# Performance work log

Measured on AMD Instinct MI355X. Metric: run time of the kernel, lower is better.

Reference implementation:

```python
import jax, jax.numpy as jnp
import numpy as np

N_NODES = 100000


def _gcn_layer(x, W, b, row, col, norm, n_nodes):
    # x: [N, Fin], W: [Fin, Fout]. GCN: A_hat @ (x W) + b with symmetric norm.
    xw = x @ W                                   # [N, Fout]
    msg = xw[row] * norm[:, None]                # [E+N, Fout] gathered messages
    agg = jax.ops.segment_sum(msg, col, num_segments=n_nodes)  # scatter-add at dst
    return agg + b


def setup_inputs() -> dict:
    key = jax.random.key(0)
    ks = jax.random.split(key, 5)
    N, E = N_NODES, 1600000
    Fin, F1, F2, C = 512, 64, 128, 40
    x = jax.random.normal(ks[0], (N, Fin), dtype=jnp.float32)
    edge_index = jax.random.randint(ks[1], (2, E), 0, N, dtype=jnp.int64)
    W1 = jax.random.normal(ks[2], (Fin, F1), dtype=jnp.float32) / np.sqrt(Fin)
    W2 = jax.random.normal(ks[3], (F1, F2), dtype=jnp.float32) / np.sqrt(F1)
    W3 = jax.random.normal(ks[4], (F2, C), dtype=jnp.float32) / np.sqrt(F2)
    return {
        "x": x, "edge_index": edge_index,
        "W1": W1, "b1": jnp.zeros((F1,), jnp.float32),
        "W2": W2, "b2": jnp.zeros((F2,), jnp.float32),
        "W3": W3, "b3": jnp.zeros((C,), jnp.float32),
    }


def reference(x, edge_index, W1, b1, W2, b2, W3, b3):
    N = x.shape[0]
    # Add self-loops (GCNConv default add_self_loops=True)
    loop = jnp.arange(N, dtype=edge_index.dtype)
    row = jnp.concatenate([edge_index[0], loop])  # source nodes
    col = jnp.concatenate([edge_index[1], loop])  # destination nodes
    # Symmetric degree normalization: deg computed at destination with self-loops
    deg = jax.ops.segment_sum(jnp.ones_like(col, dtype=x.dtype), col, num_segments=N)
    dis = jax.lax.rsqrt(deg)                      # deg >= 1 due to self-loops
    norm = dis[row] * dis[col]                    # [E+N]

    h1 = jax.nn.relu(_gcn_layer(x, W1, b1, row, col, norm, N))
    # dropout is identity (training=False)
    h2 = jax.nn.relu(_gcn_layer(h1, W2, b2, row, col, norm, N))
    h3 = _gcn_layer(h2, W3, b3, row, col, norm, N)
    return jax.nn.log_softmax(h3, axis=1)
```

## Files before the change

### kernel.cpp

```cpp
#include <hip/hip_runtime.h>
#include <math.h>


typedef __attribute__((ext_vector_type(8))) short short8;
typedef __attribute__((ext_vector_type(4))) float f32x4;

__device__ __forceinline__ unsigned short f2bf(float f) {
    unsigned int u = __float_as_uint(f);
    unsigned int r = (u + 0x7fffu + ((u >> 16) & 1u)) >> 16;
    return (unsigned short)r;
}
__device__ __forceinline__ float bflo(unsigned int u) { return __uint_as_float(u << 16); }
__device__ __forceinline__ float bfhi(unsigned int u) { return __uint_as_float(u & 0xffff0000u); }

__device__ __forceinline__ void wprep_one(const float* W, unsigned short* out,
                                          int KS, int FOUT, int t) {
    int i = t & 7;
    int l = (t >> 3) & 63;
    int g = t >> 9;
    int ks = g % KS;
    int nt = g / KS;
    int k = ks * 32 + (l >> 4) * 8 + i;
    int c = nt * 16 + (l & 15);
    out[t] = (c < FOUT) ? f2bf(W[(size_t)k * FOUT + c]) : (unsigned short)0;
}

__global__ void prep_kernel(const float* __restrict__ W1, const float* __restrict__ W2,
                            const float* __restrict__ W3,
                            unsigned short* __restrict__ Wf1, unsigned short* __restrict__ Wf2,
                            unsigned short* __restrict__ Wf3,
                            int* __restrict__ cnt, int* __restrict__ fillc, int N) {
    int t = blockIdx.x * 256 + threadIdx.x;
    if (t < 32768)       wprep_one(W1, Wf1, 16, 64, t);
    else if (t < 40960)  wprep_one(W2, Wf2, 2, 128, t - 32768);
    else if (t < 47104)  wprep_one(W3, Wf3, 4, 40, t - 40960);
    if (t < N) cnt[t] = 0;
    else if (t < 2 * N) fillc[t - N] = 0;
}

__global__ void count_kernel(const int* __restrict__ col, int* __restrict__ cnt, int E) {
    int e = blockIdx.x * 256 + threadIdx.x;
    if (e < E) atomicAdd(&cnt[col[e]], 1);
}

__global__ void scan1_kernel(const int* __restrict__ cnt, int* __restrict__ out,
                             int* __restrict__ bsums, int n) {
    __shared__ int s[1024];
    int i = blockIdx.x * 1024 + threadIdx.x;
    int v = (i < n) ? cnt[i] : 0;
    s[threadIdx.x] = v;
    __syncthreads();
    for (int off = 1; off < 1024; off <<= 1) {
        int t = 0;
        if ((int)threadIdx.x >= off) t = s[threadIdx.x - off];
        __syncthreads();
        if ((int)threadIdx.x >= off) s[threadIdx.x] += t;
        __syncthreads();
    }
    if (i < n) out[i] = s[threadIdx.x] - v;
    if (threadIdx.x == 1023) bsums[blockIdx.x] = s[1023];
}

__global__ void scan2_kernel(int* bsums, int nb) {
    __shared__ int s[128];
    int v = ((int)threadIdx.x < nb) ? bsums[threadIdx.x] : 0;
    s[threadIdx.x] = v;
    __syncthreads();
    for (int off = 1; off < 128; off <<= 1) {
        int t = 0;
        if ((int)threadIdx.x >= off) t = s[threadIdx.x - off];
        __syncthreads();
        if ((int)threadIdx.x >= off) s[threadIdx.x] += t;
        __syncthreads();
    }
    if ((int)threadIdx.x < nb) bsums[threadIdx.x] = s[threadIdx.x] - v;
}

__global__ void scan3d_kernel(int* __restrict__ ptr, const int* __restrict__ bsums,
                              const int* __restrict__ cnt, float* __restrict__ dis,
                              int n, int E) {
    int i = blockIdx.x * 1024 + threadIdx.x;
    if (i < n) {
        ptr[i] += bsums[blockIdx.x];
        dis[i] = rsqrtf((float)(cnt[i] + 1));
    }
    if (i == 0) ptr[n] = E;
}

__global__ void fill_kernel(const int* __restrict__ row, const int* __restrict__ col,
                            const int* __restrict__ ptr, int* __restrict__ fillc,
                            const float* __restrict__ dis, uint2* __restrict__ csr_en, int E) {
    int e = blockIdx.x * 256 + threadIdx.x;
    if (e < E) {
        int c = col[e];
        int r = row[e];
        int p = ptr[c] + atomicAdd(&fillc[c], 1);
        uint2 en;
        en.x = (unsigned int)r;
        en.y = __float_as_uint(dis[r] * dis[c]);
        csr_en[p] = en;
    }
}

__global__ __launch_bounds__(256) void gemm1_kernel(const float* __restrict__ Ap,
                                                    const unsigned short* __restrict__ Wf,
                                                    unsigned short* __restrict__ Y, int N) {
    __shared__ float red[3][64][17];
    const int lane = threadIdx.x & 63;
    const int wid = threadIdx.x >> 6;
    const int rbase = blockIdx.x * 16;
    const int rA = rbase + (lane & 15);
    const bool va = rA < N;
    const int khalf = lane >> 4;
    const float* base = Ap + (size_t)rA * 512 + wid * 128 + khalf * 8;

    float4 x0[4], x1[4];
#pragma unroll
    for (int s = 0; s < 4; s++) {
        const float4* arow = (const float4*)(base + s * 32);
        if (va) { x0[s] = arow[0]; x1[s] = arow[1]; }
        else    { x0[s] = make_float4(0, 0, 0, 0); x1[s] = x0[s]; }
    }

    f32x4 acc[4];
#pragma unroll
    for (int nt = 0; nt < 4; nt++)
#pragma unroll
        for (int j = 0; j < 4; j++) acc[nt][j] = 0.f;

#pragma unroll
    for (int s = 0; s < 4; s++) {
        short8 afr;
        afr[0] = (short)f2bf(x0[s].x); afr[1] = (short)f2bf(x0[s].y);
        afr[2] = (short)f2bf(x0[s].z); afr[3] = (short)f2bf(x0[s].w);
        afr[4] = (short)f2bf(x1[s].x); afr[5] = (short)f2bf(x1[s].y);
        afr[6] = (short)f2bf(x1[s].z); afr[7] = (short)f2bf(x1[s].w);
        const int ks = wid * 4 + s;
#pragma unroll
        for (int nt = 0; nt < 4; nt++) {
            short8 bfr = *(const short8*)(Wf + (((size_t)nt * 16 + ks) * 64 + lane) * 8);
            acc[nt] = __builtin_amdgcn_mfma_f32_16x16x32_bf16(afr, bfr, acc[nt], 0, 0, 0);
        }
    }

    if (wid > 0) {
#pragma unroll
        for (int nt = 0; nt < 4; nt++)
#pragma unroll
            for (int j = 0; j < 4; j++)
                red[wid - 1][lane][nt * 4 + j] = acc[nt][j];
    }
    __syncthreads();
    if (wid == 0) {
#pragma unroll
        for (int nt = 0; nt < 4; nt++)
#pragma unroll
            for (int j = 0; j < 4; j++) {
                float v = acc[nt][j];
                v += red[0][lane][nt * 4 + j];
                v += red[1][lane][nt * 4 + j];
                v += red[2][lane][nt * 4 + j];
                acc[nt][j] = v;
            }
        const int rD0 = rbase + (lane >> 4) * 4;
        const int colb = lane & 15;
#pragma unroll
        for (int nt = 0; nt < 4; nt++) {
            int c = nt * 16 + colb;
#pragma unroll
            for (int i = 0; i < 4; i++) {
                int rD = rD0 + i;
                if (rD < N) Y[(size_t)rD * 64 + c] = f2bf(acc[nt][i]);
            }
        }
    }
}

__global__ __launch_bounds__(256) void gemm23_kernel(const unsigned short* __restrict__ A,
                                                     const unsigned short* __restrict__ Wf2,
                                                     const float* __restrict__ b2,
                                                     const unsigned short* __restrict__ Wf3,
                                                     unsigned short* __restrict__ Y, int N) {
    __shared__ unsigned short hs[4][16][136];
    const int lane = threadIdx.x & 63;
    const int wid = threadIdx.x >> 6;
    const int rbase = blockIdx.x * 64 + wid * 16;
    const int rA = rbase + (lane & 15);
    const bool va = rA < N;
    const int khalf = lane >> 4;

    f32x4 acc2[8];
#pragma unroll
    for (int nt = 0; nt < 8; nt++)
#pragma unroll
        for (int j = 0; j < 4; j++) acc2[nt][j] = 0.f;

#pragma unroll
    for (int ks = 0; ks < 2; ks++) {
        short8 afr;
        if (va) afr = *(const short8*)(A + (size_t)rA * 64 + ks * 32 + khalf * 8);
        else {
#pragma unroll
            for (int j = 0; j < 8; j++) afr[j] = 0;
        }
#pragma unroll
        for (int nt = 0; nt < 8; nt++) {
            short8 bfr = *(const short8*)(Wf2 + (((size_t)nt * 2 + ks) * 64 + lane) * 8);
            acc2[nt] = __builtin_amdgcn_mfma_f32_16x16x32_bf16(afr, bfr, acc2[nt], 0, 0, 0);
        }
    }

    const int rD = (lane >> 4) * 4;
    const int colb = lane & 15;
#pragma unroll
    for (int nt = 0; nt < 8; nt++) {
        int c = nt * 16 + colb;
        float bv = b2[c];
#pragma unroll
        for (int j = 0; j < 4; j++)
            hs[wid][rD + j][c] = f2bf(fmaxf(acc2[nt][j] + bv, 0.f));
    }
    __syncthreads();

    f32x4 acc3[3];
#pragma unroll
    for (int nt = 0; nt < 3; nt++)
#pragma unroll
        for (int j = 0; j < 4; j++) acc3[nt][j] = 0.f;

    const int r = lane & 15;
#pragma unroll
    for (int ks = 0; ks < 4; ks++) {
        short8 afr = *(const short8*)&hs[wid][r][ks * 32 + khalf * 8];
#pragma unroll
        for (int nt = 0; nt < 3; nt++) {
            short8 bfr = *(const short8*)(Wf3 + (((size_t)nt * 4 + ks) * 64 + lane) * 8);
            acc3[nt] = __builtin_amdgcn_mfma_f32_16x16x32_bf16(afr, bfr, acc3[nt], 0, 0, 0);
        }
    }

#pragma unroll
    for (int nt = 0; nt < 3; nt++) {
        int c = nt * 16 + colb;
        if (c < 40) {
#pragma unroll
            for (int i = 0; i < 4; i++) {
                int rr = rbase + rD + i;
                if (rr < N) Y[(size_t)rr * 40 + c] = f2bf(acc3[nt][i]);
            }
        }
    }
}

template <bool BR>
__global__ __launch_bounds__(256) void agg64_kernel(const unsigned int* __restrict__ XW,
                                                    const float* __restrict__ bias,
                                                    const int* __restrict__ ptr,
                                                    const uint2* __restrict__ EN,
                                                    unsigned int* __restrict__ Y, int N) {
    const int lane = threadIdx.x & 63;
    const int wid = threadIdx.x >> 6;
    const int n = blockIdx.x * 4 + wid;
    if (n >= N) return;
    const int s = lane >> 3;
    const int q = lane & 7;

    const int e0 = ptr[n], e1 = ptr[n + 1];
    const float selfw = 1.0f / (float)(e1 - e0 + 1);

    float acc[8];
    if (s == 0) {
        const uint4 u = *(const uint4*)(XW + (size_t)n * 32 + q * 4);
        acc[0] = selfw * bflo(u.x); acc[1] = selfw * bfhi(u.x);
        acc[2] = selfw * bflo(u.y); acc[3] = selfw * bfhi(u.y);
        acc[4] = selfw * bflo(u.z); acc[5] = selfw * bfhi(u.z);
        acc[6] = selfw * bflo(u.w); acc[7] = selfw * bfhi(u.w);
    } else {
#pragma unroll
        for (int j = 0; j < 8; j++) acc[j] = 0.f;
    }

    for (int eb = e0; eb < e1; eb += 64) {
        int cnt = e1 - eb; if (cnt > 64) cnt = 64;
        uint2 en;
        if (lane < cnt) en = EN[eb + lane];
        else { en.x = 0; en.y = 0; }
#pragma unroll 2
        for (int k = s; k < cnt; k += 8) {
            int r = __shfl((int)en.x, k);
            float nrm = __uint_as_float((unsigned int)__shfl((int)en.y, k));
            const uint4 u = *(const uint4*)(XW + (size_t)r * 32 + q * 4);
            acc[0] += nrm * bflo(u.x); acc[1] += nrm * bfhi(u.x);
            acc[2] += nrm * bflo(u.y); acc[3] += nrm * bfhi(u.y);
            acc[4] += nrm * bflo(u.z); acc[5] += nrm * bfhi(u.z);
            acc[6] += nrm * bflo(u.w); acc[7] += nrm * bfhi(u.w);
        }
    }

#pragma unroll
    for (int off = 8; off < 64; off <<= 1)
#pragma unroll
        for (int j = 0; j < 8; j++) acc[j] += __shfl_xor(acc[j], off);

    if (lane < 8) {
        float v[8];
        if (BR) {
            const float4 b0 = *((const float4*)bias + lane * 2);
            const float4 b1 = *((const float4*)bias + lane * 2 + 1);
            v[0] = fmaxf(acc[0] + b0.x, 0.f); v[1] = fmaxf(acc[1] + b0.y, 0.f);
            v[2] = fmaxf(acc[2] + b0.z, 0.f); v[3] = fmaxf(acc[3] + b0.w, 0.f);
            v[4] = fmaxf(acc[4] + b1.x, 0.f); v[5] = fmaxf(acc[5] + b1.y, 0.f);
            v[6] = fmaxf(acc[6] + b1.z, 0.f); v[7] = fmaxf(acc[7] + b1.w, 0.f);
        } else {
#pragma unroll
            for (int j = 0; j < 8; j++) v[j] = acc[j];
        }
        uint4 o;
        o.x = (unsigned int)f2bf(v[0]) | ((unsigned int)f2bf(v[1]) << 16);
        o.y = (unsigned int)f2bf(v[2]) | ((unsigned int)f2bf(v[3]) << 16);
        o.z = (unsigned int)f2bf(v[4]) | ((unsigned int)f2bf(v[5]) << 16);
        o.w = (unsigned int)f2bf(v[6]) | ((unsigned int)f2bf(v[7]) << 16);
        *(uint4*)(Y + (size_t)n * 32 + lane * 4) = o;
    }
}

__global__ __launch_bounds__(256) void agg40lsm_kernel(const unsigned int* __restrict__ XW,
                                                       const float* __restrict__ bias,
                                                       const int* __restrict__ ptr,
                                                       const uint2* __restrict__ EN,
                                                       float* __restrict__ out, int N) {
    const int lane = threadIdx.x & 63;
    const int wid = threadIdx.x >> 6;
    const int n = blockIdx.x * 4 + wid;
    if (n >= N) return;
    const int s = lane >> 4;
    const int c = lane & 15;
    const bool act = (c < 10);

    const int e0 = ptr[n], e1 = ptr[n + 1];
    const float selfw = 1.0f / (float)(e1 - e0 + 1);

    float acc[4] = {0.f, 0.f, 0.f, 0.f};
    if (s == 0 && act) {
        const uint2 u = *(const uint2*)(XW + (size_t)n * 20 + c * 2);
        acc[0] = selfw * bflo(u.x); acc[1] = selfw * bfhi(u.x);
        acc[2] = selfw * bflo(u.y); acc[3] = selfw * bfhi(u.y);
    }

    for (int eb = e0; eb < e1; eb += 64) {
        int cnt = e1 - eb; if (cnt > 64) cnt = 64;
        uint2 en;
        if (lane < cnt) en = EN[eb + lane];
        else { en.x = 0; en.y = 0; }
#pragma unroll 2
        for (int k = s; k < cnt; k += 4) {
            int r = __shfl((int)en.x, k);
            float nrm = __uint_as_float((unsigned int)__shfl((int)en.y, k));
            if (act) {
                const uint2 u = *(const uint2*)(XW + (size_t)r * 20 + c * 2);
                acc[0] += nrm * bflo(u.x); acc[1] += nrm * bfhi(u.x);
                acc[2] += nrm * bflo(u.y); acc[3] += nrm * bfhi(u.y);
            }
        }
    }

#pragma unroll
    for (int off = 16; off < 64; off <<= 1)
#pragma unroll
        for (int j = 0; j < 4; j++) acc[j] += __shfl_xor(acc[j], off);

    float v[4];
    float m = -INFINITY;
    if (lane < 16 && act) {
        const float4 b = *((const float4*)bias + c);
        v[0] = acc[0] + b.x; v[1] = acc[1] + b.y;
        v[2] = acc[2] + b.z; v[3] = acc[3] + b.w;
        m = fmaxf(fmaxf(v[0], v[1]), fmaxf(v[2], v[3]));
    }
#pragma unroll
    for (int off = 32; off; off >>= 1) m = fmaxf(m, __shfl_xor(m, off));
    float ex = 0.f;
    if (lane < 16 && act)
        ex = expf(v[0] - m) + expf(v[1] - m) + expf(v[2] - m) + expf(v[3] - m);
#pragma unroll
    for (int off = 32; off; off >>= 1) ex += __shfl_xor(ex, off);
    float ls = logf(ex);
    if (lane < 16 && act) {
        float4 o;
        o.x = v[0] - m - ls; o.y = v[1] - m - ls;
        o.z = v[2] - m - ls; o.w = v[3] - m - ls;
        *(float4*)(out + (size_t)n * 40 + c * 4) = o;
    }
}


extern "C" void kernel_launch(void* const* d_in, const int* in_sizes, int n_in,
                              void* d_out, int out_size, void* d_ws, size_t ws_size,
                              hipStream_t stream) {
    const float* x  = (const float*)d_in[0];
    const int*   ei = (const int*)d_in[1];
    const float* W1 = (const float*)d_in[2];
    const float* b1 = (const float*)d_in[3];
    const float* W2 = (const float*)d_in[4];
    const float* b2 = (const float*)d_in[5];
    const float* W3 = (const float*)d_in[6];
    const float* b3 = (const float*)d_in[7];
    const int N = in_sizes[0] / 512;
    const int E = in_sizes[1] / 2;
    const int* row = ei;
    const int* col = ei + E;

    char* p = (char*)d_ws;
    auto alloc = [&](size_t bytes) {
        void* r = (void*)p;
        p += (bytes + 255) & ~(size_t)255;
        return r;
    };
    float* dis    = (float*)alloc((size_t)N * 4);
    int*   cnt    = (int*)alloc((size_t)N * 4);
    int*   ptr    = (int*)alloc((size_t)(N + 1) * 4);
    int*   fillc  = (int*)alloc((size_t)N * 4);
    int*   bsums  = (int*)alloc(1024);
    uint2* csr_en = (uint2*)alloc((size_t)E * 8);
    unsigned short* Wf1 = (unsigned short*)alloc(4 * 16 * 64 * 8 * 2);
    unsigned short* Wf2 = (unsigned short*)alloc(8 * 2 * 64 * 8 * 2);
    unsigned short* Wf3 = (unsigned short*)alloc(3 * 4 * 64 * 8 * 2);
    unsigned short* xw1 = (unsigned short*)alloc((size_t)N * 64 * 2);
    unsigned short* h1  = (unsigned short*)alloc((size_t)N * 64 * 2);
    unsigned short* a2  = (unsigned short*)alloc((size_t)N * 64 * 2);
    unsigned short* xw3 = (unsigned short*)alloc((size_t)N * 40 * 2);
    float* out = (float*)d_out;

    prep_kernel<<<(2 * N + 255) / 256, 256, 0, stream>>>(W1, W2, W3, Wf1, Wf2, Wf3,
                                                         cnt, fillc, N);

    const int cgrid = (E + 255) / 256;
    count_kernel<<<cgrid, 256, 0, stream>>>(col, cnt, E);

    gemm1_kernel<<<(N + 15) / 16, 256, 0, stream>>>(x, Wf1, xw1, N);

    int nb = (N + 1023) / 1024;
    scan1_kernel<<<nb, 1024, 0, stream>>>(cnt, ptr, bsums, N);
    scan2_kernel<<<1, 128, 0, stream>>>(bsums, nb);
    scan3d_kernel<<<nb, 1024, 0, stream>>>(ptr, bsums, cnt, dis, N, E);
    fill_kernel<<<cgrid, 256, 0, stream>>>(row, col, ptr, fillc, dis, csr_en, E);

    const int ngrid = (N + 3) / 4;
    const int ggrid = (N + 63) / 64;

    agg64_kernel<true><<<ngrid, 256, 0, stream>>>((const unsigned int*)xw1, b1, ptr, csr_en,
                                                  (unsigned int*)h1, N);
    agg64_kernel<false><<<ngrid, 256, 0, stream>>>((const unsigned int*)h1, nullptr, ptr, csr_en,
                                                   (unsigned int*)a2, N);
    gemm23_kernel<<<ggrid, 256, 0, stream>>>(a2, Wf2, b2, Wf3, xw3, N);
    agg40lsm_kernel<<<ngrid, 256, 0, stream>>>((const unsigned int*)xw3, b3, ptr, csr_en, out, N);
}
```

Before: 374.6 us.

## Restructure gemm1 to stage 64-row bf16 tiles in LDS with double buffering

The first-layer GEMM previously split K across four waves per 16-row block and reduced partial sums through shared memory. It now gives each block 64 rows, one 16-row slice per wave over the full K. Each K chunk of x is loaded with coalesced float4 reads, converted to bf16 and stored in a double-buffered LDS tile. This removes the cross-wave reduction and reuses each W fragment across more rows, at the cost of more LDS traffic and a barrier per chunk.

```diff
diff --git a/kernel.cpp b/kernel.cpp
--- a/kernel.cpp
+++ b/kernel.cpp
@@ -105,22 +105,13 @@
 __global__ __launch_bounds__(256) void gemm1_kernel(const float* __restrict__ Ap,
                                                     const unsigned short* __restrict__ Wf,
                                                     unsigned short* __restrict__ Y, int N) {
-    __shared__ float red[3][64][17];
-    const int lane = threadIdx.x & 63;
-    const int wid = threadIdx.x >> 6;
-    const int rbase = blockIdx.x * 16;
-    const int rA = rbase + (lane & 15);
-    const bool va = rA < N;
+    __shared__ unsigned short As[2][64][136];
+    const int t = threadIdx.x;
+    const int lane = t & 63;
+    const int wid = t >> 6;
+    const int rbase = blockIdx.x * 64;
+    const int fr = lane & 15;
     const int khalf = lane >> 4;
-    const float* base = Ap + (size_t)rA * 512 + wid * 128 + khalf * 8;
-
-    float4 x0[4], x1[4];
-#pragma unroll
-    for (int s = 0; s < 4; s++) {
-        const float4* arow = (const float4*)(base + s * 32);
-        if (va) { x0[s] = arow[0]; x1[s] = arow[1]; }
-        else    { x0[s] = make_float4(0, 0, 0, 0); x1[s] = x0[s]; }
-    }
 
     f32x4 acc[4];
 #pragma unroll
@@ -128,50 +119,48 @@
 #pragma unroll
         for (int j = 0; j < 4; j++) acc[nt][j] = 0.f;
 
-#pragma unroll
-    for (int s = 0; s < 4; s++) {
-        short8 afr;
-        afr[0] = (short)f2bf(x0[s].x); afr[1] = (short)f2bf(x0[s].y);
-        afr[2] = (short)f2bf(x0[s].z); afr[3] = (short)f2bf(x0[s].w);
-        afr[4] = (short)f2bf(x1[s].x); afr[5] = (short)f2bf(x1[s].y);
-        afr[6] = (short)f2bf(x1[s].z); afr[7] = (short)f2bf(x1[s].w);
-        const int ks = wid * 4 + s;
-#pragma unroll
-        for (int nt = 0; nt < 4; nt++) {
-            short8 bfr = *(const short8*)(Wf + (((size_t)nt * 16 + ks) * 64 + lane) * 8);
-            acc[nt] = __builtin_amdgcn_mfma_f32_16x16x32_bf16(afr, bfr, acc[nt], 0, 0, 0);
-        }
-    }
-
-    if (wid > 0) {
-#pragma unroll
-        for (int nt = 0; nt < 4; nt++)
-#pragma unroll
-            for (int j = 0; j < 4; j++)
-                red[wid - 1][lane][nt * 4 + j] = acc[nt][j];
-    }
+    auto stage = [&](int buf, int c) {
+#pragma unroll
+        for (int rd = 0; rd < 8; rd++) {
+            int u = t + rd * 256;
+            int row = u >> 5;
+            int q = u & 31;
+            int gr = rbase + row; if (gr > N - 1) gr = N - 1;
+            float4 v = *(const float4*)(Ap + (size_t)gr * 512 + c * 128 + q * 4);
+            uint2 w;
+            w.x = (unsigned int)f2bf(v.x) | ((unsigned int)f2bf(v.y) << 16);
+            w.y = (unsigned int)f2bf(v.z) | ((unsigned int)f2bf(v.w) << 16);
+            *(uint2*)&As[buf][row][q * 4] = w;
+        }
+    };
+
+    stage(0, 0);
     __syncthreads();
-    if (wid == 0) {
-#pragma unroll
-        for (int nt = 0; nt < 4; nt++)
-#pragma unroll
-            for (int j = 0; j < 4; j++) {
-                float v = acc[nt][j];
-                v += red[0][lane][nt * 4 + j];
-                v += red[1][lane][nt * 4 + j];
-                v += red[2][lane][nt * 4 + j];
-                acc[nt][j] = v;
+#pragma unroll
+    for (int c = 0; c < 4; c++) {
+        if (c < 3) stage((c + 1) & 1, c + 1);
+#pragma unroll
+        for (int ks = 0; ks < 4; ks++) {
+            short8 afr = *(const short8*)&As[c & 1][wid * 16 + fr][ks * 32 + khalf * 8];
+            const int ksg = c * 4 + ks;
+#pragma unroll
+            for (int nt = 0; nt < 4; nt++) {
+                short8 bfr = *(const short8*)(Wf + (((size_t)nt * 16 + ksg) * 64 + lane) * 8);
+                acc[nt] = __builtin_amdgcn_mfma_f32_16x16x32_bf16(afr, bfr, acc[nt], 0, 0, 0);
             }
-        const int rD0 = rbase + (lane >> 4) * 4;
-        const int colb = lane & 15;
-#pragma unroll
-        for (int nt = 0; nt < 4; nt++) {
-            int c = nt * 16 + colb;
-#pragma unroll
-            for (int i = 0; i < 4; i++) {
-                int rD = rD0 + i;
-                if (rD < N) Y[(size_t)rD * 64 + c] = f2bf(acc[nt][i]);
-            }
+        }
+        __syncthreads();
+    }
+
+    const int rD0 = rbase + wid * 16 + (lane >> 4) * 4;
+    const int colb = lane & 15;
+#pragma unroll
+    for (int nt = 0; nt < 4; nt++) {
+        int c = nt * 16 + colb;
+#pragma unroll
+        for (int i = 0; i < 4; i++) {
+            int rD = rD0 + i;
+            if (rD < N) Y[(size_t)rD * 64 + c] = f2bf(acc[nt][i]);
         }
     }
 }
@@ -437,7 +426,8 @@
     const int cgrid = (E + 255) / 256;
     count_kernel<<<cgrid, 256, 0, stream>>>(col, cnt, E);
 
-    gemm1_kernel<<<(N + 15) / 16, 256, 0, stream>>>(x, Wf1, xw1, N);
+    const int ggrid = (N + 63) / 64;
+    gemm1_kernel<<<ggrid, 256, 0, stream>>>(x, Wf1, xw1, N);
 
     int nb = (N + 1023) / 1024;
     scan1_kernel<<<nb, 1024, 0, stream>>>(cnt, ptr, bsums, N);
@@ -446,7 +436,6 @@
     fill_kernel<<<cgrid, 256, 0, stream>>>(row, col, ptr, fillc, dis, csr_en, E);
 
     const int ngrid = (N + 3) / 4;
-    const int ggrid = (N + 63) / 64;
 
     agg64_kernel<true><<<ngrid, 256, 0, stream>>>((const unsigned int*)xw1, b1, ptr, csr_en,
                                                   (unsigned int*)h1, N);
```

Result: faster. 364.9 us (-2.6%).
